# Performance work log

Hardware: AMD Instinct MI355X
Metric: run time of the kernel (lower is better)

Reference implementation:

```python
import jax, jax.numpy as jnp
import numpy as np

B, N, K, F, H = 4, 1024, 100, 42, 64


def setup_inputs() -> dict:
    key = jax.random.key(0)
    ks = jax.random.split(key, 10)
    return {
        "image": jax.random.normal(ks[0], (B, N, F), jnp.float32),
        "dfeat": jax.random.normal(ks[1], (B, N, K, F, 3), jnp.float32) * 0.1,
        "neighbor": jax.random.randint(ks[2], (B, N, K), 0, N + 1, jnp.int32),
        "Egroup_weight": jax.random.uniform(ks[3], (B, N, N), jnp.float32),
        "divider": jnp.ones((B, N), jnp.float32),
        # fitting-net params (single atom type), cfg [F, H, H, 1], tanh
        "W1": jax.random.normal(ks[4], (F, H), jnp.float32) * 0.1,
        "b1": jnp.zeros((H,), jnp.float32),
        "W2": jax.random.normal(ks[5], (H, H), jnp.float32) * 0.1,
        "b2": jnp.zeros((H,), jnp.float32),
        "W3": jax.random.normal(ks[6], (H, 1), jnp.float32) * 0.1,
        "b3": jnp.zeros((1,), jnp.float32),
    }


def reference(image, dfeat, neighbor, Egroup_weight, divider, W1, b1, W2, b2, W3, b3):
    b, n, f = image.shape
    k = neighbor.shape[-1]

    def energy(x):  # per-atom energy: [..., F] -> [...]
        h = jnp.tanh(x @ W1 + b1)
        h = jnp.tanh(h @ W2 + b2)
        return (h @ W3 + b3)[..., 0]

    Ei = energy(image)                                   # [B, N]
    # dEi/dFeat: each Ei depends only on its own feature row, so grad of sum
    # gives the per-atom Jacobian rows (the autograd=True f_FC path).
    dE = jax.grad(lambda x: energy(x).sum())(image)      # [B, N, F]
    Etot = jnp.sum(Ei, axis=1)                           # [B]

    # Fortran 1-based neighbor indices; row 0 of the padded table is zeros
    # (neighbor==0 means "no neighbor").
    dE_pad = jnp.concatenate([jnp.zeros((b, 1, f), dE.dtype), dE], axis=1)  # [B, N+1, F]
    flat = dE_pad.reshape(b * (n + 1), f)
    offs = jnp.repeat(jnp.arange(b, dtype=jnp.int32) * (n + 1), n * k)
    idx = neighbor.reshape(-1).astype(jnp.int32) + offs
    dEi_nb = flat[idx].reshape(b, n, k, f)               # gather   [B, N, K, F]
    # Force[b,i,:] = sum_j dE[neighbor(i,j)] . dfeat[b,i,j]  (reduce over K, F)
    Force = jnp.einsum('bnkf,bnkfd->bnd', dEi_nb, dfeat)  # [B, N, 3]
    return Etot, Ei, Force
```

## Files before the change

### kernel.cpp

```cpp
#include <hip/hip_runtime.h>

#define B 4
#define N 1024
#define K 100
#define F 42
#define H 64

#define PAIRS (K * F)
#define MF4   (PAIRS * 3 / 4)
#define QP    (PAIRS / 4)

#define APW 4
#define NWV 4
#define APB (APW * NWV)
#define PW  68

typedef float f32x4 __attribute__((ext_vector_type(4)));

__device__ __forceinline__ float rl(float v, int l) {
    return __int_as_float(__builtin_amdgcn_readlane(__float_as_int(v), l));
}

__global__ __launch_bounds__(256, 1) void mlp_kernel(
    const float* __restrict__ image,
    const float* __restrict__ W1, const float* __restrict__ b1,
    const float* __restrict__ W2, const float* __restrict__ b2,
    const float* __restrict__ W3, const float* __restrict__ b3,
    float* __restrict__ Ei, float* __restrict__ dE)
{
    __shared__ __align__(16) float W1s[H][PW];
    __shared__ __align__(16) float W2s[H][PW];

    const int tid  = threadIdx.x;
    const int lane = tid & 63;
    const int wv   = tid >> 6;
    const int aw   = blockIdx.x * APB + wv * APW;

    for (int idx = tid; idx < H * H; idx += 256) {
        const int r = idx >> 6, c = idx & 63;
        W1s[r][c] = (r < F) ? W1[idx] : 0.0f;
        W2s[r][c] = W2[idx];
    }
    __syncthreads();

    float w1c[F];
    #pragma unroll
    for (int f = 0; f < F; ++f) w1c[f] = W1s[f][lane];
    float w2c[H];
    #pragma unroll
    for (int j = 0; j < H; ++j) w2c[j] = W2s[j][lane];
    f32x4 w2r[H / 4];
    #pragma unroll
    for (int i = 0; i < H / 4; ++i) w2r[i] = *(const f32x4*)&W2s[lane][4 * i];
    f32x4 w1r[H / 4];
    #pragma unroll
    for (int i = 0; i < H / 4; ++i) w1r[i] = *(const f32x4*)&W1s[lane][4 * i];

    float x[APW];
    #pragma unroll
    for (int a = 0; a < APW; ++a)
        x[a] = (lane < F) ? image[(size_t)(aw + a) * F + lane] : 0.0f;

    float acc[APW];
    {
        const float bb = b1[lane];
        #pragma unroll
        for (int a = 0; a < APW; ++a) acc[a] = bb;
    }
    #pragma unroll
    for (int f = 0; f < F; ++f) {
        #pragma unroll
        for (int a = 0; a < APW; ++a)
            acc[a] = fmaf(rl(x[a], f), w1c[f], acc[a]);
    }
    float h1l[APW];
    #pragma unroll
    for (int a = 0; a < APW; ++a) h1l[a] = tanhf(acc[a]);

    {
        const float bb = b2[lane];
        #pragma unroll
        for (int a = 0; a < APW; ++a) acc[a] = bb;
    }
    #pragma unroll
    for (int j = 0; j < H; ++j) {
        #pragma unroll
        for (int a = 0; a < APW; ++a)
            acc[a] = fmaf(rl(h1l[a], j), w2c[j], acc[a]);
    }

    const float w3    = W3[lane];
    const float bias3 = b3[0];
    float g2l[APW];
    #pragma unroll
    for (int a = 0; a < APW; ++a) {
        const float h2 = tanhf(acc[a]);
        g2l[a] = w3 * (1.0f - h2 * h2);
        float t = h2 * w3;
        #pragma unroll
        for (int off = 32; off > 0; off >>= 1) t += __shfl_down(t, off);
        if (lane == 0) Ei[aw + a] = t + bias3;
    }

    float g1l[APW];
    {
        float s[APW] = {0.f, 0.f, 0.f, 0.f};
        #pragma unroll
        for (int i = 0; i < H; ++i) {
            const float w = w2r[i >> 2][i & 3];
            #pragma unroll
            for (int a = 0; a < APW; ++a)
                s[a] = fmaf(rl(g2l[a], i), w, s[a]);
        }
        #pragma unroll
        for (int a = 0; a < APW; ++a)
            g1l[a] = s[a] * (1.0f - h1l[a] * h1l[a]);
    }

    float dx[APW] = {0.f, 0.f, 0.f, 0.f};
    #pragma unroll
    for (int i = 0; i < H; ++i) {
        const float w = w1r[i >> 2][i & 3];
        #pragma unroll
        for (int a = 0; a < APW; ++a)
            dx[a] = fmaf(rl(g1l[a], i), w, dx[a]);
    }
    if (lane < F) {
        #pragma unroll
        for (int a = 0; a < APW; ++a)
            dE[(size_t)(aw + a) * F + lane] = dx[a];
    }
}

__global__ __launch_bounds__(256) void force_kernel(
    const float* __restrict__ dE, const float* __restrict__ dfeat,
    const int* __restrict__ neighbor, const float* __restrict__ Ei,
    float* __restrict__ force, float* __restrict__ Etot)
{
    __shared__ int   nsh[K];
    __shared__ float red[4][3];

    const int tid  = threadIdx.x;
    const int bid  = blockIdx.x;
    const int lane = tid & 63, wave = tid >> 6;

    if (bid >= B * N) {
        const int b = bid - B * N;
        float s = 0.0f;
        for (int i = tid; i < N; i += 256) s += Ei[b * N + i];
        #pragma unroll
        for (int off = 32; off > 0; off >>= 1) s += __shfl_down(s, off);
        if (lane == 0) red[wave][0] = s;
        __syncthreads();
        if (tid == 0)
            Etot[b] = (red[0][0] + red[1][0]) + (red[2][0] + red[3][0]);
        return;
    }

    const int bn = bid;
    const int b  = bn >> 10;

    if (tid < K) nsh[tid] = neighbor[bn * K + tid];
    __syncthreads();

    const f32x4* df4 = (const f32x4*)dfeat + (size_t)bn * MF4;
    const float* dEb = dE + (size_t)b * (N * F);

    float fx = 0.0f, fy = 0.0f, fz = 0.0f;

    #pragma unroll 1
    for (int it = 0; it < 4; ++it) {
        const int p4 = it * 256 + tid;
        const int p  = 4 * p4;
        const f32x4 d0 = df4[3 * p4 + 0];
        const f32x4 d1 = df4[3 * p4 + 1];
        const f32x4 d2 = df4[3 * p4 + 2];
        float e[4];
        #pragma unroll
        for (int q = 0; q < 4; ++q) {
            const int pp = p + q;
            const int k  = pp / F;
            const int f  = pp - k * F;
            const int nb = nsh[k];
            e[q] = (nb > 0) ? dEb[(nb - 1) * F + f] : 0.0f;
        }
        fx = fmaf(e[0], d0.x, fx); fy = fmaf(e[0], d0.y, fy); fz = fmaf(e[0], d0.z, fz);
        fx = fmaf(e[1], d0.w, fx); fy = fmaf(e[1], d1.x, fy); fz = fmaf(e[1], d1.y, fz);
        fx = fmaf(e[2], d1.z, fx); fy = fmaf(e[2], d1.w, fy); fz = fmaf(e[2], d2.x, fz);
        fx = fmaf(e[3], d2.y, fx); fy = fmaf(e[3], d2.z, fy); fz = fmaf(e[3], d2.w, fz);
    }
    if (tid < QP - 1024) {
        const int p4 = 1024 + tid;
        const int p  = 4 * p4;
        const f32x4 d0 = df4[3 * p4 + 0];
        const f32x4 d1 = df4[3 * p4 + 1];
        const f32x4 d2 = df4[3 * p4 + 2];
        float e[4];
        #pragma unroll
        for (int q = 0; q < 4; ++q) {
            const int pp = p + q;
            const int k  = pp / F;
            const int f  = pp - k * F;
            const int nb = nsh[k];
            e[q] = (nb > 0) ? dEb[(nb - 1) * F + f] : 0.0f;
        }
        fx = fmaf(e[0], d0.x, fx); fy = fmaf(e[0], d0.y, fy); fz = fmaf(e[0], d0.z, fz);
        fx = fmaf(e[1], d0.w, fx); fy = fmaf(e[1], d1.x, fy); fz = fmaf(e[1], d1.y, fz);
        fx = fmaf(e[2], d1.z, fx); fy = fmaf(e[2], d1.w, fy); fz = fmaf(e[2], d2.x, fz);
        fx = fmaf(e[3], d2.y, fx); fy = fmaf(e[3], d2.z, fy); fz = fmaf(e[3], d2.w, fz);
    }

    #pragma unroll
    for (int off = 32; off > 0; off >>= 1) {
        fx += __shfl_down(fx, off);
        fy += __shfl_down(fy, off);
        fz += __shfl_down(fz, off);
    }
    if (lane == 0) { red[wave][0] = fx; red[wave][1] = fy; red[wave][2] = fz; }
    __syncthreads();
    if (tid == 0) {
        force[bn * 3 + 0] = (red[0][0] + red[1][0]) + (red[2][0] + red[3][0]);
        force[bn * 3 + 1] = (red[0][1] + red[1][1]) + (red[2][1] + red[3][1]);
        force[bn * 3 + 2] = (red[0][2] + red[1][2]) + (red[2][2] + red[3][2]);
    }
}

extern "C" void kernel_launch(void* const* d_in, const int* in_sizes, int n_in,
                              void* d_out, int out_size, void* d_ws, size_t ws_size,
                              hipStream_t stream)
{
    const float* image    = (const float*)d_in[0];
    const float* dfeat    = (const float*)d_in[1];
    const int*   neighbor = (const int*)d_in[2];
    const float* W1 = (const float*)d_in[5];
    const float* b1 = (const float*)d_in[6];
    const float* W2 = (const float*)d_in[7];
    const float* b2 = (const float*)d_in[8];
    const float* W3 = (const float*)d_in[9];
    const float* b3 = (const float*)d_in[10];

    float* out   = (float*)d_out;
    float* Etot  = out;
    float* Ei    = out + B;
    float* Force = out + B + B * N;
    float* dE    = (float*)d_ws;

    mlp_kernel<<<(B * N) / APB, 256, 0, stream>>>(image, W1, b1, W2, b2, W3, b3, Ei, dE);
    force_kernel<<<B * N + B, 256, 0, stream>>>(dE, dfeat, neighbor, Ei, Force, Etot);
}
```

Measured before the change: 51.77 us.

## Read MLP weights from transposed LDS as vec4 instead of per-lane register caches

The MLP kernel stops caching full weight columns and rows in registers. It stores transposed copies of W1 and W2 in shared memory and reads them as float4 chunks inside each layer loop. Each dot product now uses four independent accumulators to shorten the FMA dependency chain. Work per wave drops from 4 atoms to 2 and the block grows to 512 threads, which gives more waves and lower register pressure, at the cost of more LDS traffic and twice the shared memory per block. The force kernel, which likely dominates runtime, is unchanged.

```diff
diff --git a/kernel.cpp b/kernel.cpp
--- a/kernel.cpp
+++ b/kernel.cpp
@@ -10,9 +10,10 @@
 #define MF4   (PAIRS * 3 / 4)
 #define QP    (PAIRS / 4)
 
-#define APW 4
-#define NWV 4
+#define APW 2
+#define NWV 8
 #define APB (APW * NWV)
+#define BT  (NWV * 64)
 #define PW  68
 
 typedef float f32x4 __attribute__((ext_vector_type(4)));
@@ -21,13 +22,15 @@
     return __int_as_float(__builtin_amdgcn_readlane(__float_as_int(v), l));
 }
 
-__global__ __launch_bounds__(256, 1) void mlp_kernel(
+__global__ __launch_bounds__(BT) void mlp_kernel(
     const float* __restrict__ image,
     const float* __restrict__ W1, const float* __restrict__ b1,
     const float* __restrict__ W2, const float* __restrict__ b2,
     const float* __restrict__ W3, const float* __restrict__ b3,
     float* __restrict__ Ei, float* __restrict__ dE)
 {
+    __shared__ __align__(16) float W1T[H][PW];
+    __shared__ __align__(16) float W2T[H][PW];
     __shared__ __align__(16) float W1s[H][PW];
     __shared__ __align__(16) float W2s[H][PW];
 
@@ -36,65 +39,72 @@
     const int wv   = tid >> 6;
     const int aw   = blockIdx.x * APB + wv * APW;
 
-    for (int idx = tid; idx < H * H; idx += 256) {
+    for (int idx = tid; idx < H * PW; idx += BT) {
+        ((float*)W1T)[idx] = 0.0f;
+        ((float*)W1s)[idx] = 0.0f;
+    }
+    __syncthreads();
+    for (int idx = tid; idx < F * H; idx += BT) {
         const int r = idx >> 6, c = idx & 63;
-        W1s[r][c] = (r < F) ? W1[idx] : 0.0f;
+        W1s[r][c] = W1[idx];
+        W1T[c][r] = W1[idx];
+    }
+    for (int idx = tid; idx < H * H; idx += BT) {
+        const int r = idx >> 6, c = idx & 63;
         W2s[r][c] = W2[idx];
-    }
-    __syncthreads();
-
-    float w1c[F];
-    #pragma unroll
-    for (int f = 0; f < F; ++f) w1c[f] = W1s[f][lane];
-    float w2c[H];
-    #pragma unroll
-    for (int j = 0; j < H; ++j) w2c[j] = W2s[j][lane];
-    f32x4 w2r[H / 4];
-    #pragma unroll
-    for (int i = 0; i < H / 4; ++i) w2r[i] = *(const f32x4*)&W2s[lane][4 * i];
-    f32x4 w1r[H / 4];
-    #pragma unroll
-    for (int i = 0; i < H / 4; ++i) w1r[i] = *(const f32x4*)&W1s[lane][4 * i];
+        W2T[c][r] = W2[idx];
+    }
+    __syncthreads();
 
     float x[APW];
     #pragma unroll
     for (int a = 0; a < APW; ++a)
         x[a] = (lane < F) ? image[(size_t)(aw + a) * F + lane] : 0.0f;
 
-    float acc[APW];
-    {
-        const float bb = b1[lane];
-        #pragma unroll
-        for (int a = 0; a < APW; ++a) acc[a] = bb;
-    }
-    #pragma unroll
-    for (int f = 0; f < F; ++f) {
-        #pragma unroll
-        for (int a = 0; a < APW; ++a)
-            acc[a] = fmaf(rl(x[a], f), w1c[f], acc[a]);
-    }
+    float p[APW][4];
+    #pragma unroll
+    for (int a = 0; a < APW; ++a)
+        #pragma unroll
+        for (int t = 0; t < 4; ++t) p[a][t] = 0.0f;
+    #pragma unroll
+    for (int fc = 0; fc < 11; ++fc) {
+        const f32x4 w = *(const f32x4*)&W1T[lane][4 * fc];
+        #pragma unroll
+        for (int a = 0; a < APW; ++a) {
+            p[a][0] = fmaf(rl(x[a], 4 * fc + 0), w.x, p[a][0]);
+            p[a][1] = fmaf(rl(x[a], 4 * fc + 1), w.y, p[a][1]);
+            p[a][2] = fmaf(rl(x[a], 4 * fc + 2), w.z, p[a][2]);
+            p[a][3] = fmaf(rl(x[a], 4 * fc + 3), w.w, p[a][3]);
+        }
+    }
+    const float bb1 = b1[lane];
     float h1l[APW];
     #pragma unroll
-    for (int a = 0; a < APW; ++a) h1l[a] = tanhf(acc[a]);
-
-    {
-        const float bb = b2[lane];
-        #pragma unroll
-        for (int a = 0; a < APW; ++a) acc[a] = bb;
-    }
-    #pragma unroll
-    for (int j = 0; j < H; ++j) {
-        #pragma unroll
-        for (int a = 0; a < APW; ++a)
-            acc[a] = fmaf(rl(h1l[a], j), w2c[j], acc[a]);
-    }
-
+    for (int a = 0; a < APW; ++a)
+        h1l[a] = tanhf((p[a][0] + p[a][1]) + (p[a][2] + p[a][3]) + bb1);
+
+    #pragma unroll
+    for (int a = 0; a < APW; ++a)
+        #pragma unroll
+        for (int t = 0; t < 4; ++t) p[a][t] = 0.0f;
+    #pragma unroll
+    for (int jc = 0; jc < H / 4; ++jc) {
+        const f32x4 w = *(const f32x4*)&W2T[lane][4 * jc];
+        #pragma unroll
+        for (int a = 0; a < APW; ++a) {
+            p[a][0] = fmaf(rl(h1l[a], 4 * jc + 0), w.x, p[a][0]);
+            p[a][1] = fmaf(rl(h1l[a], 4 * jc + 1), w.y, p[a][1]);
+            p[a][2] = fmaf(rl(h1l[a], 4 * jc + 2), w.z, p[a][2]);
+            p[a][3] = fmaf(rl(h1l[a], 4 * jc + 3), w.w, p[a][3]);
+        }
+    }
+    const float bb2   = b2[lane];
     const float w3    = W3[lane];
     const float bias3 = b3[0];
     float g2l[APW];
     #pragma unroll
     for (int a = 0; a < APW; ++a) {
-        const float h2 = tanhf(acc[a]);
+        const float h2 = tanhf((p[a][0] + p[a][1]) + (p[a][2] + p[a][3]) + bb2);
         g2l[a] = w3 * (1.0f - h2 * h2);
         float t = h2 * w3;
         #pragma unroll
@@ -102,33 +112,46 @@
         if (lane == 0) Ei[aw + a] = t + bias3;
     }
 
+    #pragma unroll
+    for (int a = 0; a < APW; ++a)
+        #pragma unroll
+        for (int t = 0; t < 4; ++t) p[a][t] = 0.0f;
+    #pragma unroll
+    for (int ic = 0; ic < H / 4; ++ic) {
+        const f32x4 w = *(const f32x4*)&W2s[lane][4 * ic];
+        #pragma unroll
+        for (int a = 0; a < APW; ++a) {
+            p[a][0] = fmaf(rl(g2l[a], 4 * ic + 0), w.x, p[a][0]);
+            p[a][1] = fmaf(rl(g2l[a], 4 * ic + 1), w.y, p[a][1]);
+            p[a][2] = fmaf(rl(g2l[a], 4 * ic + 2), w.z, p[a][2]);
+            p[a][3] = fmaf(rl(g2l[a], 4 * ic + 3), w.w, p[a][3]);
+        }
+    }
     float g1l[APW];
-    {
-        float s[APW] = {0.f, 0.f, 0.f, 0.f};
-        #pragma unroll
-        for (int i = 0; i < H; ++i) {
-            const float w = w2r[i >> 2][i & 3];
-            #pragma unroll
-            for (int a = 0; a < APW; ++a)
-                s[a] = fmaf(rl(g2l[a], i), w, s[a]);
-        }
+    #pragma unroll
+    for (int a = 0; a < APW; ++a)
+        g1l[a] = ((p[a][0] + p[a][1]) + (p[a][2] + p[a][3])) * (1.0f - h1l[a] * h1l[a]);
+
+    #pragma unroll
+    for (int a = 0; a < APW; ++a)
+        #pragma unroll
+        for (int t = 0; t < 4; ++t) p[a][t] = 0.0f;
+    #pragma unroll
+    for (int ic = 0; ic < H / 4; ++ic) {
+        const f32x4 w = *(const f32x4*)&W1s[lane][4 * ic];
+        #pragma unroll
+        for (int a = 0; a < APW; ++a) {
+            p[a][0] = fmaf(rl(g1l[a], 4 * ic + 0), w.x, p[a][0]);
+            p[a][1] = fmaf(rl(g1l[a], 4 * ic + 1), w.y, p[a][1]);
+            p[a][2] = fmaf(rl(g1l[a], 4 * ic + 2), w.z, p[a][2]);
+            p[a][3] = fmaf(rl(g1l[a], 4 * ic + 3), w.w, p[a][3]);
+        }
+    }
+    if (lane < F) {
         #pragma unroll
         for (int a = 0; a < APW; ++a)
-            g1l[a] = s[a] * (1.0f - h1l[a] * h1l[a]);
-    }
-
-    float dx[APW] = {0.f, 0.f, 0.f, 0.f};
-    #pragma unroll
-    for (int i = 0; i < H; ++i) {
-        const float w = w1r[i >> 2][i & 3];
-        #pragma unroll
-        for (int a = 0; a < APW; ++a)
-            dx[a] = fmaf(rl(g1l[a], i), w, dx[a]);
-    }
-    if (lane < F) {
-        #pragma unroll
-        for (int a = 0; a < APW; ++a)
-            dE[(size_t)(aw + a) * F + lane] = dx[a];
+            dE[(size_t)(aw + a) * F + lane] =
+                (p[a][0] + p[a][1]) + (p[a][2] + p[a][3]);
     }
 }
 
@@ -245,6 +268,6 @@
     float* Force = out + B + B * N;
     float* dE    = (float*)d_ws;
 
-    mlp_kernel<<<(B * N) / APB, 256, 0, stream>>>(image, W1, b1, W2, b2, W3, b3, Ei, dE);
+    mlp_kernel<<<(B * N) / APB, BT, 0, stream>>>(image, W1, b1, W2, b2, W3, b3, Ei, dE);
     force_kernel<<<B * N + B, 256, 0, stream>>>(dE, dfeat, neighbor, Ei, Force, Etot);
 }
```

Result: faster. 45.54 us (-12.0%).
